# Optimization experiments

Measured on AMD Instinct MI355X. Metric: run time of the kernel, lower is better.

The kernel has to match this reference:

```python
import jax, jax.numpy as jnp
import numpy as np


def setup_inputs() -> dict:
    key = jax.random.key(0)
    k1, k2 = jax.random.split(key)
    B, P, D = 32, 512, 384
    x = jax.random.normal(k1, (B, P, D), dtype=jnp.float32)
    duration = jax.random.randint(k2, (B, P), 0, 5, dtype=jnp.int32)
    return {"x": x, "duration": duration, "max_len": 2048}


def reference(x, duration, max_len):
    # x: [B, P, D], duration: [B, P] int, max_len: python int
    B, P, D = x.shape
    dur = duration.astype(jnp.int32)
    ends = jnp.cumsum(dur, axis=1)          # [B, P] exclusive end offsets per phoneme
    mel_lens = ends[:, -1]                   # [B] total frames per utterance
    t = jnp.arange(max_len, dtype=jnp.int32)
    # frame t belongs to phoneme i where ends[i-1] <= t < ends[i]
    idx = jax.vmap(lambda e: jnp.searchsorted(e, t, side='right'))(ends)  # [B, T]
    idx = jnp.clip(idx, 0, P - 1)
    out = jnp.take_along_axis(x, idx[..., None], axis=1)  # [B, T, D]
    mask = (t[None, :] < mel_lens[:, None])[..., None]     # zero out padding frames
    out = jnp.where(mask, out, jnp.zeros((), dtype=x.dtype))
    return out, mel_lens
```

## Files before the change

### kernel.cpp

```cpp
#include <hip/hip_runtime.h>

#define LR_B      32
#define LR_P      512
#define LR_D      384
#define LR_MAXLEN 2048
#define LR_V4     (LR_D / 4)
#define LR_FPB    32
#define LR_F4PB   (LR_FPB * LR_V4)
#define LR_THREADS 256
#define LR_F4PT   (LR_F4PB / LR_THREADS)

#define LR_CHUNKS  (LR_MAXLEN / LR_FPB)
#define LR_GBLOCKS (LR_B * LR_CHUNKS)
#define LR_NXCD    8
#define LR_CPX     (LR_GBLOCKS / LR_NXCD)

typedef float f32x4 __attribute__((ext_vector_type(4)));

__global__ __launch_bounds__(LR_THREADS) void lr_fused(
    const int*   __restrict__ dur,
    const f32x4* __restrict__ x4,
    f32x4*       __restrict__ out4,
    float*       __restrict__ mel_out)
{
    const int bid = blockIdx.x;
    const int lb  = (bid & (LR_NXCD - 1)) * LR_CPX + (bid >> 3);

    const int b    = lb >> 6;
    const int c    = lb & 63;
    const int base = c * LR_FPB;

    const int tid  = threadIdx.x;
    const int lane = tid & 63;
    const int wid  = tid >> 6;

    __shared__ int smem_idx[LR_FPB];
    __shared__ int wsum[LR_THREADS / 64];

    if (tid < LR_FPB) smem_idx[tid] = -1;

    const int2 d2 = ((const int2*)(dur + b * LR_P))[tid];
    const int  e0 = d2.x, e1 = d2.y;
    int s = e0 + e1;

    #pragma unroll
    for (int off = 1; off < 64; off <<= 1) {
        int u = __shfl_up(s, off, 64);
        if (lane >= off) s += u;
    }
    if (lane == 63) wsum[wid] = s;
    __syncthreads();

    int woff = 0, total = 0;
    #pragma unroll
    for (int i = 0; i < LR_THREADS / 64; ++i) {
        int w = wsum[i];
        woff  += (i < wid) ? w : 0;
        total += w;
    }
    const int ends1  = s + woff;
    const int ends0  = ends1 - e1;
    const int start0 = ends0 - e0;

    {
        int lo = max(start0, base), hi = min(ends0, base + LR_FPB);
        for (int f = lo; f < hi; ++f) smem_idx[f - base] = 2 * tid;
        lo = max(ends0, base);  hi = min(ends1, base + LR_FPB);
        for (int f = lo; f < hi; ++f) smem_idx[f - base] = 2 * tid + 1;
    }
    if (c == 0 && tid == 0) mel_out[b] = (float)total;
    __syncthreads();

    const f32x4* xb    = x4 + (size_t)b * LR_P * LR_V4;
    f32x4*       ob    = out4 + ((size_t)b * LR_MAXLEN + base) * LR_V4;
    #pragma unroll
    for (int k = 0; k < LR_F4PT; ++k) {
        const unsigned j     = tid + k * LR_THREADS;
        const unsigned frame = j / LR_V4;
        const unsigned v     = j - frame * LR_V4;
        const int p = smem_idx[frame];
        f32x4 val;
        if (p >= 0) {
            val = xb[(unsigned)p * LR_V4 + v];
        } else {
            val = (f32x4){0.f, 0.f, 0.f, 0.f};
        }
        __builtin_nontemporal_store(val, &ob[j]);
    }
}

extern "C" void kernel_launch(void* const* d_in, const int* in_sizes, int n_in,
                              void* d_out, int out_size, void* d_ws, size_t ws_size,
                              hipStream_t stream)
{
    const float* x   = (const float*)d_in[0];
    const int*   dur = (const int*)d_in[1];

    float* out = (float*)d_out;
    float* mel = out + (size_t)LR_B * LR_MAXLEN * LR_D;

    lr_fused<<<LR_GBLOCKS, LR_THREADS, 0, stream>>>(
        dur, (const f32x4*)x, (f32x4*)out, mel);
}
```

Before: 25.23 us.

## Double frames per block, use one phoneme per thread, batch gathers unconditionally

Each block now covers 64 frames with 512 threads, so each thread scans one phoneme duration instead of two. The per-block prefix scan is amortized over twice as many output frames. The gather loop is split into phases: index loads, then unconditional loads (padding frames clamped to row 0), then stores with zeros selected. This issues all loads up front for more memory-level parallelism. The cost is redundant loads for padding frames and more registers per thread.

```diff
diff --git a/kernel.cpp b/kernel.cpp
--- a/kernel.cpp
+++ b/kernel.cpp
@@ -5,9 +5,9 @@
 #define LR_D      384
 #define LR_MAXLEN 2048
 #define LR_V4     (LR_D / 4)
-#define LR_FPB    32
+#define LR_FPB    64
+#define LR_THREADS 512
 #define LR_F4PB   (LR_FPB * LR_V4)
-#define LR_THREADS 256
 #define LR_F4PT   (LR_F4PB / LR_THREADS)
 
 #define LR_CHUNKS  (LR_MAXLEN / LR_FPB)
@@ -26,8 +26,8 @@
     const int bid = blockIdx.x;
     const int lb  = (bid & (LR_NXCD - 1)) * LR_CPX + (bid >> 3);
 
-    const int b    = lb >> 6;
-    const int c    = lb & 63;
+    const int b    = lb >> 5;
+    const int c    = lb & 31;
     const int base = c * LR_FPB;
 
     const int tid  = threadIdx.x;
@@ -39,9 +39,8 @@
 
     if (tid < LR_FPB) smem_idx[tid] = -1;
 
-    const int2 d2 = ((const int2*)(dur + b * LR_P))[tid];
-    const int  e0 = d2.x, e1 = d2.y;
-    int s = e0 + e1;
+    const int e = dur[b * LR_P + tid];
+    int s = e;
 
     #pragma unroll
     for (int off = 1; off < 64; off <<= 1) {
@@ -58,34 +57,41 @@
         woff  += (i < wid) ? w : 0;
         total += w;
     }
-    const int ends1  = s + woff;
-    const int ends0  = ends1 - e1;
-    const int start0 = ends0 - e0;
+    const int end   = s + woff;
+    const int start = end - e;
 
     {
-        int lo = max(start0, base), hi = min(ends0, base + LR_FPB);
-        for (int f = lo; f < hi; ++f) smem_idx[f - base] = 2 * tid;
-        lo = max(ends0, base);  hi = min(ends1, base + LR_FPB);
-        for (int f = lo; f < hi; ++f) smem_idx[f - base] = 2 * tid + 1;
+        const int lo = max(start, base), hi = min(end, base + LR_FPB);
+        for (int f = lo; f < hi; ++f) smem_idx[f - base] = tid;
     }
     if (c == 0 && tid == 0) mel_out[b] = (float)total;
     __syncthreads();
 
-    const f32x4* xb    = x4 + (size_t)b * LR_P * LR_V4;
-    f32x4*       ob    = out4 + ((size_t)b * LR_MAXLEN + base) * LR_V4;
+    const f32x4* xb = x4 + (size_t)b * LR_P * LR_V4;
+    f32x4*       ob = out4 + ((size_t)b * LR_MAXLEN + base) * LR_V4;
+
+    int      pr[LR_F4PT];
+    unsigned vv[LR_F4PT];
     #pragma unroll
     for (int k = 0; k < LR_F4PT; ++k) {
         const unsigned j     = tid + k * LR_THREADS;
         const unsigned frame = j / LR_V4;
-        const unsigned v     = j - frame * LR_V4;
-        const int p = smem_idx[frame];
-        f32x4 val;
-        if (p >= 0) {
-            val = xb[(unsigned)p * LR_V4 + v];
-        } else {
-            val = (f32x4){0.f, 0.f, 0.f, 0.f};
-        }
-        __builtin_nontemporal_store(val, &ob[j]);
+        vv[k] = j - frame * LR_V4;
+        pr[k] = smem_idx[frame];
+    }
+
+    f32x4 vals[LR_F4PT];
+    #pragma unroll
+    for (int k = 0; k < LR_F4PT; ++k) {
+        const unsigned row = (unsigned)max(pr[k], 0);
+        vals[k] = xb[row * LR_V4 + vv[k]];
+    }
+
+    const f32x4 zero = (f32x4){0.f, 0.f, 0.f, 0.f};
+    #pragma unroll
+    for (int k = 0; k < LR_F4PT; ++k) {
+        f32x4 v = (pr[k] < 0) ? zero : vals[k];
+        __builtin_nontemporal_store(v, &ob[tid + k * LR_THREADS]);
     }
 }
 
```

Measured after the change: 25.28 us. About the same (+0.2%).
